# Optimization experiments

Measured on AMD Instinct MI355X. Metric: run time of the kernel, lower is better.

## Reference

```python
import jax, jax.numpy as jnp
import numpy as np

DIM = 768
NUM_HEADS = 12
HEAD_DIM = DIM // NUM_HEADS
SCALE = HEAD_DIM ** (-0.5)
LN_EPS = 1e-5


def setup_inputs() -> dict:
    key = jax.random.key(0)
    ks = jax.random.split(key, 8)
    B, K, C = 4, 2048, DIM
    return {
        "x": jax.random.normal(ks[0], (B, K, C), jnp.float32),
        "pos_embed": jax.random.normal(ks[1], (B, K, C), jnp.float32),
        "rel_pos_bias": jax.random.normal(ks[2], (B, K, K), jnp.float32),
        "ln_g": jnp.ones((C,), jnp.float32),
        "ln_b": jnp.zeros((C,), jnp.float32),
        "qkv_w": jax.random.normal(ks[3], (C, 3 * C), jnp.float32) * 0.02,
        "qkv_b": jnp.zeros((3 * C,), jnp.float32),
        "proj_w": jax.random.normal(ks[4], (C, C), jnp.float32) * 0.02,
        "proj_b": jnp.zeros((C,), jnp.float32),
    }


def _layernorm(x, g, b):
    mu = jnp.mean(x, axis=-1, keepdims=True)
    var = jnp.mean(jnp.square(x - mu), axis=-1, keepdims=True)
    return (x - mu) * jax.lax.rsqrt(var + LN_EPS) * g + b


def reference(x, pos_embed, rel_pos_bias, ln_g, ln_b, qkv_w, qkv_b, proj_w, proj_b):
    B, K, C = x.shape
    H, D = NUM_HEADS, HEAD_DIM
    xp = _layernorm(x, ln_g, ln_b) + pos_embed
    qkv = xp @ qkv_w + qkv_b                      # [B,K,3C]
    qkv = qkv.reshape(B, K, 3, H, D)
    q = jnp.transpose(qkv[:, :, 0], (0, 2, 1, 3))  # [B,H,K,D]
    k = jnp.transpose(qkv[:, :, 1], (0, 2, 1, 3))
    v = jnp.transpose(qkv[:, :, 2], (0, 2, 1, 3))
    attn = jnp.einsum("bhqd,bhkd->bhqk", q, k) * SCALE
    attn = attn + rel_pos_bias[:, None, :, :]
    attn = jax.nn.softmax(attn, axis=-1)
    out = jnp.einsum("bhqk,bhkd->bhqd", attn, v)   # [B,H,K,D]
    out = jnp.transpose(out, (0, 2, 1, 3)).reshape(B, K, C)
    # DropPath(0.1) is identity in eval mode
    return out @ proj_w + proj_b
```

## Files before the change

kernel.cpp:

```cpp
#include <hip/hip_runtime.h>
#include <hip/hip_bf16.h>
#include <stdint.h>

typedef __attribute__((ext_vector_type(4))) float f32x4;
typedef __attribute__((ext_vector_type(16))) float f32x16;
typedef __attribute__((ext_vector_type(8))) short s16x8;
typedef __attribute__((ext_vector_type(4))) short s16x4;
typedef uint16_t u16;

#define DEV __device__ __forceinline__

static DEV u16 f2bf(float f) {
  union { float f; uint32_t u; } v; v.f = f;
  uint32_t r = v.u + 0x7fffu + ((v.u >> 16) & 1u);
  return (u16)(r >> 16);
}

static DEV uint32_t cvt_pk_bf16(float lo, float hi) {
  uint32_t r;
  asm("v_cvt_pk_bf16_f32 %0, %1, %2" : "=v"(r) : "v"(lo), "v"(hi));
  return r;
}

#define GLD_LDS16(gp, lp) __builtin_amdgcn_global_load_lds( \
    (const __attribute__((address_space(1))) void*)(gp),    \
    (__attribute__((address_space(3))) void*)(lp), 16, 0, 0)

__global__ __launch_bounds__(256) void k_ln(
    const float* __restrict__ x, const float* __restrict__ pos,
    const float* __restrict__ g, const float* __restrict__ be,
    u16* __restrict__ xp) {
  int row = blockIdx.x;
  size_t base = (size_t)row * 768;
  int t = threadIdx.x;
  float v0 = x[base + t], v1 = x[base + t + 256], v2 = x[base + t + 512];
  float s = v0 + v1 + v2;
  float ss = v0 * v0 + v1 * v1 + v2 * v2;
#pragma unroll
  for (int off = 1; off < 64; off <<= 1) {
    s += __shfl_xor(s, off);
    ss += __shfl_xor(ss, off);
  }
  __shared__ float red[8];
  int wave = t >> 6, lane = t & 63;
  if (lane == 0) { red[wave] = s; red[4 + wave] = ss; }
  __syncthreads();
  float tot = red[0] + red[1] + red[2] + red[3];
  float tss = red[4] + red[5] + red[6] + red[7];
  float mu = tot * (1.0f / 768.0f);
  float var = tss * (1.0f / 768.0f) - mu * mu;
  float rs = rsqrtf(var + 1e-5f);
  float vv[3] = {v0, v1, v2};
#pragma unroll
  for (int i = 0; i < 3; ++i) {
    int c = t + i * 256;
    float val = (vv[i] - mu) * rs * g[c] + be[c] + pos[base + c];
    xp[base + c] = f2bf(val);
  }
}

__global__ __launch_bounds__(256) void k_tr(
    const float* __restrict__ in, u16* __restrict__ out, int K, int N) {
  __shared__ float tile[32][33];
  int n0 = blockIdx.x * 32, k0 = blockIdx.y * 32;
  int tx = threadIdx.x & 31, ty = threadIdx.x >> 5;
#pragma unroll
  for (int r = ty; r < 32; r += 8)
    tile[r][tx] = in[(size_t)(k0 + r) * N + n0 + tx];
  __syncthreads();
#pragma unroll
  for (int r = ty; r < 32; r += 8)
    out[(size_t)(n0 + r) * K + k0 + tx] = f2bf(tile[tx][r]);
}

__global__ __launch_bounds__(256) void k_gemm_qkv(
    const u16* __restrict__ A, const u16* __restrict__ Bt,
    const float* __restrict__ bias, u16* __restrict__ qkv,
    u16* __restrict__ vtg) {
  __shared__ u16 Al[128 * 64];
  __shared__ u16 Bl[128 * 64];
  const size_t BHKD = (size_t)48 * 2048 * 64;
  int mt = blockIdx.x, nt = blockIdx.y;
  int t = threadIdx.x, wave = t >> 6, lane = t & 63;
  int lr = lane & 15, lg = lane >> 4;
  f32x4 acc[4][4];
#pragma unroll
  for (int i = 0; i < 4; ++i)
#pragma unroll
    for (int j = 0; j < 4; ++j) acc[i][j] = (f32x4){0.f, 0.f, 0.f, 0.f};
  const size_t Ab = (size_t)mt * 128 * 768;
  const size_t Bb = (size_t)nt * 128 * 768;
  int wr = (wave >> 1) * 64, wc = (wave & 1) * 64;
  for (int kt = 0; kt < 12; ++kt) {
#pragma unroll
    for (int c = 0; c < 4; ++c) {
      int q = c * 256 + t;
      int row = q >> 3, ch = q & 7;
      int sc = ch ^ (row & 7);
      GLD_LDS16(A + Ab + (size_t)row * 768 + kt * 64 + sc * 8,
                &Al[(size_t)(c * 256 + wave * 64) * 8]);
      GLD_LDS16(Bt + Bb + (size_t)row * 768 + kt * 64 + sc * 8,
                &Bl[(size_t)(c * 256 + wave * 64) * 8]);
    }
    __syncthreads();
#pragma unroll
    for (int ki = 0; ki < 2; ++ki) {
      s16x8 af[4], bf[4];
#pragma unroll
      for (int mi = 0; mi < 4; ++mi)
        af[mi] = *(const s16x8*)&Al[(wr + mi * 16 + lr) * 64 +
                                    (((ki * 4 + lg) ^ (lr & 7)) * 8)];
#pragma unroll
      for (int ni = 0; ni < 4; ++ni)
        bf[ni] = *(const s16x8*)&Bl[(wc + ni * 16 + lr) * 64 +
                                    (((ki * 4 + lg) ^ (lr & 7)) * 8)];
#pragma unroll
      for (int mi = 0; mi < 4; ++mi)
#pragma unroll
        for (int ni = 0; ni < 4; ++ni)
          acc[mi][ni] = __builtin_amdgcn_mfma_f32_16x16x32_bf16(
              af[mi], bf[ni], acc[mi][ni], 0, 0, 0);
    }
    __syncthreads();
  }
#pragma unroll
  for (int ni = 0; ni < 4; ++ni) {
    int col = wc + ni * 16 + lr;
    int n = nt * 128 + col;
    int which = n / 768, cc = n % 768;
    int h = cc >> 6, d = cc & 63;
    float bs = bias[n];
    if (which == 2) {
#pragma unroll
      for (int mi = 0; mi < 4; ++mi) {
        int m0 = mt * 128 + wr + mi * 16 + lg * 4;
        int b = m0 >> 11, kp0 = m0 & 2047;
        s16x4 o4;
#pragma unroll
        for (int j = 0; j < 4; ++j) o4[j] = (short)f2bf(acc[mi][ni][j] + bs);
        *(s16x4*)&vtg[((size_t)(b * 12 + h) * 64 + d) * 2048 + kp0] = o4;
      }
    } else {
#pragma unroll
      for (int mi = 0; mi < 4; ++mi) {
#pragma unroll
        for (int j = 0; j < 4; ++j) {
          int row = wr + mi * 16 + lg * 4 + j;
          int m = mt * 128 + row;
          int b = m >> 11, kp = m & 2047;
          size_t dst = (size_t)which * BHKD +
                       (((size_t)b * 12 + h) * 2048 + kp) * 64 + d;
          qkv[dst] = f2bf(acc[mi][ni][j] + bs);
        }
      }
    }
  }
}

#define STAGE_KV(KB, VB, ktt) do {                                          \
  _Pragma("unroll")                                                         \
  for (int c_ = 0; c_ < 2; ++c_) {                                          \
    int q_ = c_ * 256 + t; int r_ = q_ >> 3, ch_ = q_ & 7;                  \
    int sc_ = ch_ ^ (r_ & 7);                                               \
    int gk_ = (r_ & 0x33) | ((r_ & 4) << 1) | ((r_ & 8) >> 1);              \
    GLD_LDS16(Kg + ((size_t)((ktt) * 64 + gk_)) * 64 + sc_ * 8,             \
              &KB[(c_ * 256 + wave * 64) * 8]);                             \
    GLD_LDS16(Vt + (size_t)r_ * 2048 + (ktt) * 64 + sc_ * 8,                \
              &VB[(c_ * 256 + wave * 64) * 8]);                             \
  }                                                                         \
} while (0)

#define COMPUTE_TILE(KB, VB, ktt) do {                                      \
  f32x4 bv_[8];                                                             \
  _Pragma("unroll")                                                         \
  for (int kv_ = 0; kv_ < 2; ++kv_) {                                       \
    _Pragma("unroll")                                                       \
    for (int rn_ = 0; rn_ < 2; ++rn_) {                                     \
      const float* bp_ = Bgl + (ktt) * 64 + kv_ * 32 + rn_ * 16;            \
      bv_[(kv_ * 2 + rn_) * 2]     = *(const f32x4*)bp_;                    \
      bv_[(kv_ * 2 + rn_) * 2 + 1] = *(const f32x4*)(bp_ + 4);              \
    }                                                                       \
  }                                                                         \
  f32x16 sa_[2];                                                            \
  _Pragma("unroll")                                                         \
  for (int r = 0; r < 16; ++r) { sa_[0][r] = 0.f; sa_[1][r] = 0.f; }        \
  _Pragma("unroll")                                                         \
  for (int ki = 0; ki < 4; ++ki) {                                          \
    _Pragma("unroll")                                                       \
    for (int kv_ = 0; kv_ < 2; ++kv_) {                                     \
      s16x8 kf = *(const s16x8*)&KB[(kv_ * 32 + l31) * 64 +                 \
                                    (((ki * 2 + hi) ^ (l31 & 7)) * 8)];     \
      sa_[kv_] = __builtin_amdgcn_mfma_f32_32x32x16_bf16(kf, qf[ki],        \
                                                         sa_[kv_], 0, 0, 0);\
    }                                                                       \
  }                                                                         \
  float p_[32];                                                             \
  _Pragma("unroll")                                                         \
  for (int kv_ = 0; kv_ < 2; ++kv_)                                         \
    _Pragma("unroll")                                                       \
    for (int r = 0; r < 16; ++r)                                            \
      p_[kv_ * 16 + r] = exp2f(                                             \
          __builtin_fmaf(sa_[kv_][r], 0.125f,                               \
              bv_[kv_ * 4 + (r >> 3) * 2 + ((r >> 2) & 1)][r & 3]) *        \
          1.442695041f);                                                    \
  float tm_[16];                                                            \
  _Pragma("unroll")                                                         \
  for (int i = 0; i < 16; ++i) tm_[i] = p_[i] + p_[i + 16];                 \
  _Pragma("unroll")                                                         \
  for (int off = 8; off >= 1; off >>= 1)                                    \
    _Pragma("unroll")                                                       \
    for (int i = 0; i < off; ++i) tm_[i] += tm_[i + off];                   \
  l_run += tm_[0];                                                          \
  union { uint32_t u[4]; s16x8 v; } pa_[4];                                 \
  _Pragma("unroll")                                                         \
  for (int s = 0; s < 4; ++s)                                               \
    _Pragma("unroll")                                                       \
    for (int w = 0; w < 4; ++w)                                             \
      pa_[s].u[w] = cvt_pk_bf16(p_[(s >> 1) * 16 + (s & 1) * 8 + 2 * w],    \
                                p_[(s >> 1) * 16 + (s & 1) * 8 + 2 * w + 1]);\
  _Pragma("unroll")                                                         \
  for (int s = 0; s < 4; ++s) {                                             \
    _Pragma("unroll")                                                       \
    for (int dt = 0; dt < 2; ++dt) {                                        \
      s16x8 vf = *(const s16x8*)&VB[(dt * 32 + l31) * 64 +                  \
                                    (((s * 2 + hi) ^ (l31 & 7)) * 8)];      \
      oacc[dt] = __builtin_amdgcn_mfma_f32_32x32x16_bf16(vf, pa_[s].v,      \
                                                         oacc[dt], 0, 0, 0);\
    }                                                                       \
  }                                                                         \
} while (0)

__global__ __launch_bounds__(256, 3) void k_attn(
    const u16* __restrict__ qkv, const u16* __restrict__ vtg,
    const float* __restrict__ bias, u16* __restrict__ ctx) {
  __shared__ u16 Kl0[64 * 64], Vl0[64 * 64];
  __shared__ u16 Kl1[64 * 64], Vl1[64 * 64];
  int bid = blockIdx.x;
  int swz = (bid & 7) * 96 + (bid >> 3);
  int h = swz % 12;
  int bq = swz / 12;
  int qt = bq & 15;
  int b = bq >> 4;
  int bh = b * 12 + h;
  int t = threadIdx.x, wave = t >> 6, lane = t & 63;
  int l31 = lane & 31, hi = lane >> 5;
  const size_t BHKD = (size_t)48 * 2048 * 64;
  const u16* Q = qkv + (size_t)bh * 2048 * 64;
  const u16* Kg = Q + BHKD;
  const u16* Vt = vtg + (size_t)bh * 64 * 2048;
  int qrow = qt * 128 + wave * 32 + l31;
  const float* Bgl = bias + ((size_t)b * 2048 + qrow) * 2048 + hi * 8;
  s16x8 qf[4];
#pragma unroll
  for (int ki = 0; ki < 4; ++ki)
    qf[ki] = *(const s16x8*)&Q[(size_t)qrow * 64 + ki * 16 + hi * 8];
  f32x16 oacc[2];
#pragma unroll
  for (int r = 0; r < 16; ++r) { oacc[0][r] = 0.f; oacc[1][r] = 0.f; }
  float l_run = 0.f;

  STAGE_KV(Kl0, Vl0, 0);
  __syncthreads();
  for (int kt = 0; kt < 32; kt += 2) {
    STAGE_KV(Kl1, Vl1, kt + 1);
    COMPUTE_TILE(Kl0, Vl0, kt);
    __syncthreads();
    if (kt + 2 < 32) STAGE_KV(Kl0, Vl0, kt + 2);
    COMPUTE_TILE(Kl1, Vl1, kt + 1);
    __syncthreads();
  }
  float l_tot = l_run + __shfl_xor(l_run, 32);
  float inv = 1.0f / l_tot;
  size_t obase = ((size_t)b * 2048 + qrow) * 768 + h * 64;
#pragma unroll
  for (int dt = 0; dt < 2; ++dt) {
#pragma unroll
    for (int g = 0; g < 4; ++g) {
      s16x4 o4;
#pragma unroll
      for (int j = 0; j < 4; ++j)
        o4[j] = (short)f2bf(oacc[dt][g * 4 + j] * inv);
      *(s16x4*)&ctx[obase + dt * 32 + g * 8 + hi * 4] = o4;
    }
  }
}

__global__ __launch_bounds__(256) void k_gemm_proj(
    const u16* __restrict__ A, const u16* __restrict__ Bt,
    const float* __restrict__ bias, float* __restrict__ out) {
  __shared__ u16 Al[128 * 64];
  __shared__ u16 Bl[128 * 64];
  int mt = blockIdx.x, nt = blockIdx.y;
  int t = threadIdx.x, wave = t >> 6, lane = t & 63;
  int lr = lane & 15, lg = lane >> 4;
  f32x4 acc[4][4];
#pragma unroll
  for (int i = 0; i < 4; ++i)
#pragma unroll
    for (int j = 0; j < 4; ++j) acc[i][j] = (f32x4){0.f, 0.f, 0.f, 0.f};
  const size_t Ab = (size_t)mt * 128 * 768;
  const size_t Bb = (size_t)nt * 128 * 768;
  int wr = (wave >> 1) * 64, wc = (wave & 1) * 64;
  for (int kt = 0; kt < 12; ++kt) {
#pragma unroll
    for (int c = 0; c < 4; ++c) {
      int q = c * 256 + t;
      int row = q >> 3, ch = q & 7;
      int sc = ch ^ (row & 7);
      GLD_LDS16(A + Ab + (size_t)row * 768 + kt * 64 + sc * 8,
                &Al[(size_t)(c * 256 + wave * 64) * 8]);
      GLD_LDS16(Bt + Bb + (size_t)row * 768 + kt * 64 + sc * 8,
                &Bl[(size_t)(c * 256 + wave * 64) * 8]);
    }
    __syncthreads();
#pragma unroll
    for (int ki = 0; ki < 2; ++ki) {
      s16x8 af[4], bf[4];
#pragma unroll
      for (int mi = 0; mi < 4; ++mi)
        af[mi] = *(const s16x8*)&Al[(wr + mi * 16 + lr) * 64 +
                                    (((ki * 4 + lg) ^ (lr & 7)) * 8)];
#pragma unroll
      for (int ni = 0; ni < 4; ++ni)
        bf[ni] = *(const s16x8*)&Bl[(wc + ni * 16 + lr) * 64 +
                                    (((ki * 4 + lg) ^ (lr & 7)) * 8)];
#pragma unroll
      for (int mi = 0; mi < 4; ++mi)
#pragma unroll
        for (int ni = 0; ni < 4; ++ni)
          acc[mi][ni] = __builtin_amdgcn_mfma_f32_16x16x32_bf16(
              af[mi], bf[ni], acc[mi][ni], 0, 0, 0);
    }
    __syncthreads();
  }
#pragma unroll
  for (int ni = 0; ni < 4; ++ni) {
    int col = wc + ni * 16 + lr;
    int n = nt * 128 + col;
    float bs = bias[n];
#pragma unroll
    for (int mi = 0; mi < 4; ++mi) {
#pragma unroll
      for (int j = 0; j < 4; ++j) {
        int row = wr + mi * 16 + lg * 4 + j;
        out[(size_t)(mt * 128 + row) * 768 + n] = acc[mi][ni][j] + bs;
      }
    }
  }
}

extern "C" void kernel_launch(void* const* d_in, const int* in_sizes, int n_in,
                              void* d_out, int out_size, void* d_ws, size_t ws_size,
                              hipStream_t stream) {
  const float* x      = (const float*)d_in[0];
  const float* pos    = (const float*)d_in[1];
  const float* bias   = (const float*)d_in[2];
  const float* ln_g   = (const float*)d_in[3];
  const float* ln_b   = (const float*)d_in[4];
  const float* qkv_w  = (const float*)d_in[5];
  const float* qkv_b  = (const float*)d_in[6];
  const float* proj_w = (const float*)d_in[7];
  const float* proj_b = (const float*)d_in[8];
  float* out = (float*)d_out;

  char* ws = (char*)d_ws;
  u16* xp      = (u16*)ws;              ws += 12582912;
  u16* qkv_wt  = (u16*)ws;              ws += 3538944;
  u16* proj_wt = (u16*)ws;              ws += 1179648;
  u16* qkvbuf  = (u16*)ws;              ws += 25165824;
  u16* ctx     = (u16*)ws;              ws += 12582912;
  u16* vtg     = (u16*)ws;              ws += 12582912;

  k_ln<<<8192, 256, 0, stream>>>(x, pos, ln_g, ln_b, xp);
  k_tr<<<dim3(72, 24), 256, 0, stream>>>(qkv_w, qkv_wt, 768, 2304);
  k_tr<<<dim3(24, 24), 256, 0, stream>>>(proj_w, proj_wt, 768, 768);
  k_gemm_qkv<<<dim3(64, 18), 256, 0, stream>>>(xp, qkv_wt, qkv_b, qkvbuf, vtg);
  k_attn<<<768, 256, 0, stream>>>(qkvbuf, vtg, bias, ctx);
  k_gemm_proj<<<dim3(64, 6), 256, 0, stream>>>(ctx, proj_wt, proj_b, out);
}
```

Baseline: 205.0 us.

## Load K/V fragments directly from global memory instead of staging through LDS

Removes the double-buffered LDS staging of K and V tiles and their barriers in the attention kernel. Each lane now reads its MFMA K and V fragments straight from global memory, relying on L1/L2 reuse across the four waves that share the same K/V tile. This eliminates LDS traffic and __syncthreads, but each wave issues its own global loads, so cache-level traffic is up to 4x higher and latency is only hidden by within-iteration ordering. The occupancy hint of 3 blocks per CU is also dropped.

Result: slower. 346.7 us (+69.1%).

```diff
diff --git a/kernel.cpp b/kernel.cpp
--- a/kernel.cpp
+++ b/kernel.cpp
@@ -157,84 +157,9 @@
   }
 }
 
-#define STAGE_KV(KB, VB, ktt) do {                                          \
-  _Pragma("unroll")                                                         \
-  for (int c_ = 0; c_ < 2; ++c_) {                                          \
-    int q_ = c_ * 256 + t; int r_ = q_ >> 3, ch_ = q_ & 7;                  \
-    int sc_ = ch_ ^ (r_ & 7);                                               \
-    int gk_ = (r_ & 0x33) | ((r_ & 4) << 1) | ((r_ & 8) >> 1);              \
-    GLD_LDS16(Kg + ((size_t)((ktt) * 64 + gk_)) * 64 + sc_ * 8,             \
-              &KB[(c_ * 256 + wave * 64) * 8]);                             \
-    GLD_LDS16(Vt + (size_t)r_ * 2048 + (ktt) * 64 + sc_ * 8,                \
-              &VB[(c_ * 256 + wave * 64) * 8]);                             \
-  }                                                                         \
-} while (0)
-
-#define COMPUTE_TILE(KB, VB, ktt) do {                                      \
-  f32x4 bv_[8];                                                             \
-  _Pragma("unroll")                                                         \
-  for (int kv_ = 0; kv_ < 2; ++kv_) {                                       \
-    _Pragma("unroll")                                                       \
-    for (int rn_ = 0; rn_ < 2; ++rn_) {                                     \
-      const float* bp_ = Bgl + (ktt) * 64 + kv_ * 32 + rn_ * 16;            \
-      bv_[(kv_ * 2 + rn_) * 2]     = *(const f32x4*)bp_;                    \
-      bv_[(kv_ * 2 + rn_) * 2 + 1] = *(const f32x4*)(bp_ + 4);              \
-    }                                                                       \
-  }                                                                         \
-  f32x16 sa_[2];                                                            \
-  _Pragma("unroll")                                                         \
-  for (int r = 0; r < 16; ++r) { sa_[0][r] = 0.f; sa_[1][r] = 0.f; }        \
-  _Pragma("unroll")                                                         \
-  for (int ki = 0; ki < 4; ++ki) {                                          \
-    _Pragma("unroll")                                                       \
-    for (int kv_ = 0; kv_ < 2; ++kv_) {                                     \
-      s16x8 kf = *(const s16x8*)&KB[(kv_ * 32 + l31) * 64 +                 \
-                                    (((ki * 2 + hi) ^ (l31 & 7)) * 8)];     \
-      sa_[kv_] = __builtin_amdgcn_mfma_f32_32x32x16_bf16(kf, qf[ki],        \
-                                                         sa_[kv_], 0, 0, 0);\
-    }                                                                       \
-  }                                                                         \
-  float p_[32];                                                             \
-  _Pragma("unroll")                                                         \
-  for (int kv_ = 0; kv_ < 2; ++kv_)                                         \
-    _Pragma("unroll")                                                       \
-    for (int r = 0; r < 16; ++r)                                            \
-      p_[kv_ * 16 + r] = exp2f(                                             \
-          __builtin_fmaf(sa_[kv_][r], 0.125f,                               \
-              bv_[kv_ * 4 + (r >> 3) * 2 + ((r >> 2) & 1)][r & 3]) *        \
-          1.442695041f);                                                    \
-  float tm_[16];                                                            \
-  _Pragma("unroll")                                                         \
-  for (int i = 0; i < 16; ++i) tm_[i] = p_[i] + p_[i + 16];                 \
-  _Pragma("unroll")                                                         \
-  for (int off = 8; off >= 1; off >>= 1)                                    \
-    _Pragma("unroll")                                                       \
-    for (int i = 0; i < off; ++i) tm_[i] += tm_[i + off];                   \
-  l_run += tm_[0];                                                          \
-  union { uint32_t u[4]; s16x8 v; } pa_[4];                                 \
-  _Pragma("unroll")                                                         \
-  for (int s = 0; s < 4; ++s)                                               \
-    _Pragma("unroll")                                                       \
-    for (int w = 0; w < 4; ++w)                                             \
-      pa_[s].u[w] = cvt_pk_bf16(p_[(s >> 1) * 16 + (s & 1) * 8 + 2 * w],    \
-                                p_[(s >> 1) * 16 + (s & 1) * 8 + 2 * w + 1]);\
-  _Pragma("unroll")                                                         \
-  for (int s = 0; s < 4; ++s) {                                             \
-    _Pragma("unroll")                                                       \
-    for (int dt = 0; dt < 2; ++dt) {                                        \
-      s16x8 vf = *(const s16x8*)&VB[(dt * 32 + l31) * 64 +                  \
-                                    (((s * 2 + hi) ^ (l31 & 7)) * 8)];      \
-      oacc[dt] = __builtin_amdgcn_mfma_f32_32x32x16_bf16(vf, pa_[s].v,      \
-                                                         oacc[dt], 0, 0, 0);\
-    }                                                                       \
-  }                                                                         \
-} while (0)
-
-__global__ __launch_bounds__(256, 3) void k_attn(
+__global__ __launch_bounds__(256) void k_attn(
     const u16* __restrict__ qkv, const u16* __restrict__ vtg,
     const float* __restrict__ bias, u16* __restrict__ ctx) {
-  __shared__ u16 Kl0[64 * 64], Vl0[64 * 64];
-  __shared__ u16 Kl1[64 * 64], Vl1[64 * 64];
   int bid = blockIdx.x;
   int swz = (bid & 7) * 96 + (bid >> 3);
   int h = swz % 12;
@@ -244,12 +169,15 @@
   int bh = b * 12 + h;
   int t = threadIdx.x, wave = t >> 6, lane = t & 63;
   int l31 = lane & 31, hi = lane >> 5;
+  int l31s = (l31 & 0x13) | ((l31 & 4) << 1) | ((l31 & 8) >> 1);
   const size_t BHKD = (size_t)48 * 2048 * 64;
   const u16* Q = qkv + (size_t)bh * 2048 * 64;
   const u16* Kg = Q + BHKD;
   const u16* Vt = vtg + (size_t)bh * 64 * 2048;
   int qrow = qt * 128 + wave * 32 + l31;
   const float* Bgl = bias + ((size_t)b * 2048 + qrow) * 2048 + hi * 8;
+  const u16* Kp0 = Kg + (size_t)l31s * 64 + hi * 8;
+  const u16* Vp0 = Vt + (size_t)l31 * 2048 + hi * 8;
   s16x8 qf[4];
 #pragma unroll
   for (int ki = 0; ki < 4; ++ki)
@@ -259,15 +187,71 @@
   for (int r = 0; r < 16; ++r) { oacc[0][r] = 0.f; oacc[1][r] = 0.f; }
   float l_run = 0.f;
 
-  STAGE_KV(Kl0, Vl0, 0);
-  __syncthreads();
-  for (int kt = 0; kt < 32; kt += 2) {
-    STAGE_KV(Kl1, Vl1, kt + 1);
-    COMPUTE_TILE(Kl0, Vl0, kt);
-    __syncthreads();
-    if (kt + 2 < 32) STAGE_KV(Kl0, Vl0, kt + 2);
-    COMPUTE_TILE(Kl1, Vl1, kt + 1);
-    __syncthreads();
+#pragma unroll 1
+  for (int kt = 0; kt < 32; ++kt) {
+    f32x4 bv_[8];
+#pragma unroll
+    for (int kv2 = 0; kv2 < 2; ++kv2) {
+#pragma unroll
+      for (int rn = 0; rn < 2; ++rn) {
+        const float* bp_ = Bgl + kt * 64 + kv2 * 32 + rn * 16;
+        bv_[(kv2 * 2 + rn) * 2]     = *(const f32x4*)bp_;
+        bv_[(kv2 * 2 + rn) * 2 + 1] = *(const f32x4*)(bp_ + 4);
+      }
+    }
+    s16x8 kf[8];
+#pragma unroll
+    for (int ki = 0; ki < 4; ++ki)
+#pragma unroll
+      for (int kv2 = 0; kv2 < 2; ++kv2)
+        kf[ki * 2 + kv2] = *(const s16x8*)(Kp0 +
+            ((size_t)kt * 64 + kv2 * 32) * 64 + ki * 16);
+    f32x16 sa_[2];
+#pragma unroll
+    for (int r = 0; r < 16; ++r) { sa_[0][r] = 0.f; sa_[1][r] = 0.f; }
+#pragma unroll
+    for (int ki = 0; ki < 4; ++ki)
+#pragma unroll
+      for (int kv2 = 0; kv2 < 2; ++kv2)
+        sa_[kv2] = __builtin_amdgcn_mfma_f32_32x32x16_bf16(
+            kf[ki * 2 + kv2], qf[ki], sa_[kv2], 0, 0, 0);
+    s16x8 vf[8];
+#pragma unroll
+    for (int s = 0; s < 4; ++s)
+#pragma unroll
+      for (int dt = 0; dt < 2; ++dt)
+        vf[s * 2 + dt] = *(const s16x8*)(Vp0 +
+            (size_t)dt * 32 * 2048 + kt * 64 + s * 16);
+    float p_[32];
+#pragma unroll
+    for (int kv2 = 0; kv2 < 2; ++kv2)
+#pragma unroll
+      for (int r = 0; r < 16; ++r)
+        p_[kv2 * 16 + r] = exp2f(
+            __builtin_fmaf(sa_[kv2][r], 0.125f,
+                bv_[kv2 * 4 + (r >> 3) * 2 + ((r >> 2) & 1)][r & 3]) *
+            1.442695041f);
+    float tm_[16];
+#pragma unroll
+    for (int i = 0; i < 16; ++i) tm_[i] = p_[i] + p_[i + 16];
+#pragma unroll
+    for (int off = 8; off >= 1; off >>= 1)
+#pragma unroll
+      for (int i = 0; i < off; ++i) tm_[i] += tm_[i + off];
+    l_run += tm_[0];
+    union { uint32_t u[4]; s16x8 v; } pa_[4];
+#pragma unroll
+    for (int s = 0; s < 4; ++s)
+#pragma unroll
+      for (int w = 0; w < 4; ++w)
+        pa_[s].u[w] = cvt_pk_bf16(p_[(s >> 1) * 16 + (s & 1) * 8 + 2 * w],
+                                  p_[(s >> 1) * 16 + (s & 1) * 8 + 2 * w + 1]);
+#pragma unroll
+    for (int s = 0; s < 4; ++s)
+#pragma unroll
+      for (int dt = 0; dt < 2; ++dt)
+        oacc[dt] = __builtin_amdgcn_mfma_f32_32x32x16_bf16(
+            vf[s * 2 + dt], pa_[s].v, oacc[dt], 0, 0, 0);
   }
   float l_tot = l_run + __shfl_xor(l_run, 32);
   float inv = 1.0f / l_tot;
```

## Split attention KV tile across two wave groups and reduce partials via LDS

Applied to the files above, without the earlier changes.

The attention block grows from 256 to 512 threads. Each group of four waves handles half of every 64-key tile, so per-wave score, exp and PV work is halved, and staging is spread over twice as many threads. The two partial outputs and row sums are combined through shared memory at the end before normalising. The goal is more waves in flight to hide latency, at the cost of extra LDS (about 17 KB), extra barriers and a final reduction, with fewer blocks able to reside per CU.

New measurement: 402.8 us. +96.5%, slower.

```diff
diff --git a/kernel.cpp b/kernel.cpp
--- a/kernel.cpp
+++ b/kernel.cpp
@@ -158,83 +158,71 @@
 }
 
 #define STAGE_KV(KB, VB, ktt) do {                                          \
-  _Pragma("unroll")                                                         \
-  for (int c_ = 0; c_ < 2; ++c_) {                                          \
-    int q_ = c_ * 256 + t; int r_ = q_ >> 3, ch_ = q_ & 7;                  \
+    int r_ = t >> 3, ch_ = t & 7;                                           \
     int sc_ = ch_ ^ (r_ & 7);                                               \
     int gk_ = (r_ & 0x33) | ((r_ & 4) << 1) | ((r_ & 8) >> 1);              \
     GLD_LDS16(Kg + ((size_t)((ktt) * 64 + gk_)) * 64 + sc_ * 8,             \
-              &KB[(c_ * 256 + wave * 64) * 8]);                             \
+              &KB[wave * 64 * 8]);                                          \
     GLD_LDS16(Vt + (size_t)r_ * 2048 + (ktt) * 64 + sc_ * 8,                \
-              &VB[(c_ * 256 + wave * 64) * 8]);                             \
+              &VB[wave * 64 * 8]);                                          \
+} while (0)
+
+#define COMPUTE_TILE(KB, VB, ktt) do {                                      \
+  f32x4 bv_[4];                                                             \
+  {                                                                         \
+    const float* bp_ = Bgl + (ktt) * 64 + kvh * 32;                         \
+    bv_[0] = *(const f32x4*)bp_;                                            \
+    bv_[1] = *(const f32x4*)(bp_ + 4);                                      \
+    bv_[2] = *(const f32x4*)(bp_ + 16);                                     \
+    bv_[3] = *(const f32x4*)(bp_ + 20);                                     \
   }                                                                         \
-} while (0)
-
-#define COMPUTE_TILE(KB, VB, ktt) do {                                      \
-  f32x4 bv_[8];                                                             \
-  _Pragma("unroll")                                                         \
-  for (int kv_ = 0; kv_ < 2; ++kv_) {                                       \
-    _Pragma("unroll")                                                       \
-    for (int rn_ = 0; rn_ < 2; ++rn_) {                                     \
-      const float* bp_ = Bgl + (ktt) * 64 + kv_ * 32 + rn_ * 16;            \
-      bv_[(kv_ * 2 + rn_) * 2]     = *(const f32x4*)bp_;                    \
-      bv_[(kv_ * 2 + rn_) * 2 + 1] = *(const f32x4*)(bp_ + 4);              \
-    }                                                                       \
+  f32x16 sa_;                                                               \
+  _Pragma("unroll")                                                         \
+  for (int r = 0; r < 16; ++r) sa_[r] = 0.f;                                \
+  _Pragma("unroll")                                                         \
+  for (int ki = 0; ki < 4; ++ki) {                                          \
+    s16x8 kf = *(const s16x8*)&KB[(kvh * 32 + l31) * 64 +                   \
+                                  (((ki * 2 + hi) ^ (l31 & 7)) * 8)];       \
+    sa_ = __builtin_amdgcn_mfma_f32_32x32x16_bf16(kf, qf[ki], sa_, 0, 0, 0);\
   }                                                                         \
-  f32x16 sa_[2];                                                            \
-  _Pragma("unroll")                                                         \
-  for (int r = 0; r < 16; ++r) { sa_[0][r] = 0.f; sa_[1][r] = 0.f; }        \
-  _Pragma("unroll")                                                         \
-  for (int ki = 0; ki < 4; ++ki) {                                          \
-    _Pragma("unroll")                                                       \
-    for (int kv_ = 0; kv_ < 2; ++kv_) {                                     \
-      s16x8 kf = *(const s16x8*)&KB[(kv_ * 32 + l31) * 64 +                 \
-                                    (((ki * 2 + hi) ^ (l31 & 7)) * 8)];     \
-      sa_[kv_] = __builtin_amdgcn_mfma_f32_32x32x16_bf16(kf, qf[ki],        \
-                                                         sa_[kv_], 0, 0, 0);\
-    }                                                                       \
-  }                                                                         \
-  float p_[32];                                                             \
-  _Pragma("unroll")                                                         \
-  for (int kv_ = 0; kv_ < 2; ++kv_)                                         \
-    _Pragma("unroll")                                                       \
-    for (int r = 0; r < 16; ++r)                                            \
-      p_[kv_ * 16 + r] = exp2f(                                             \
-          __builtin_fmaf(sa_[kv_][r], 0.125f,                               \
-              bv_[kv_ * 4 + (r >> 3) * 2 + ((r >> 2) & 1)][r & 3]) *        \
-          1.442695041f);                                                    \
-  float tm_[16];                                                            \
-  _Pragma("unroll")                                                         \
-  for (int i = 0; i < 16; ++i) tm_[i] = p_[i] + p_[i + 16];                 \
-  _Pragma("unroll")                                                         \
-  for (int off = 8; off >= 1; off >>= 1)                                    \
+  float p_[16];                                                             \
+  _Pragma("unroll")                                                         \
+  for (int r = 0; r < 16; ++r)                                              \
+    p_[r] = exp2f(__builtin_fmaf(sa_[r], 0.125f,                            \
+                bv_[(r >> 3) * 2 + ((r >> 2) & 1)][r & 3]) * 1.442695041f); \
+  float tm_[8];                                                             \
+  _Pragma("unroll")                                                         \
+  for (int i = 0; i < 8; ++i) tm_[i] = p_[i] + p_[i + 8];                   \
+  _Pragma("unroll")                                                         \
+  for (int off = 4; off >= 1; off >>= 1)                                    \
     _Pragma("unroll")                                                       \
     for (int i = 0; i < off; ++i) tm_[i] += tm_[i + off];                   \
   l_run += tm_[0];                                                          \
-  union { uint32_t u[4]; s16x8 v; } pa_[4];                                 \
-  _Pragma("unroll")                                                         \
-  for (int s = 0; s < 4; ++s)                                               \
+  union { uint32_t u[4]; s16x8 v; } pa_[2];                                 \
+  _Pragma("unroll")                                                         \
+  for (int s = 0; s < 2; ++s)                                               \
     _Pragma("unroll")                                                       \
     for (int w = 0; w < 4; ++w)                                             \
-      pa_[s].u[w] = cvt_pk_bf16(p_[(s >> 1) * 16 + (s & 1) * 8 + 2 * w],    \
-                                p_[(s >> 1) * 16 + (s & 1) * 8 + 2 * w + 1]);\
-  _Pragma("unroll")                                                         \
-  for (int s = 0; s < 4; ++s) {                                             \
+      pa_[s].u[w] = cvt_pk_bf16(p_[s * 8 + 2 * w], p_[s * 8 + 2 * w + 1]);  \
+  _Pragma("unroll")                                                         \
+  for (int s = 0; s < 2; ++s) {                                             \
     _Pragma("unroll")                                                       \
     for (int dt = 0; dt < 2; ++dt) {                                        \
       s16x8 vf = *(const s16x8*)&VB[(dt * 32 + l31) * 64 +                  \
-                                    (((s * 2 + hi) ^ (l31 & 7)) * 8)];      \
+                    (((kvh * 4 + s * 2 + hi) ^ (l31 & 7)) * 8)];            \
       oacc[dt] = __builtin_amdgcn_mfma_f32_32x32x16_bf16(vf, pa_[s].v,      \
                                                          oacc[dt], 0, 0, 0);\
     }                                                                       \
   }                                                                         \
 } while (0)
 
-__global__ __launch_bounds__(256, 3) void k_attn(
+__global__ __launch_bounds__(512, 6) void k_attn(
     const u16* __restrict__ qkv, const u16* __restrict__ vtg,
     const float* __restrict__ bias, u16* __restrict__ ctx) {
   __shared__ u16 Kl0[64 * 64], Vl0[64 * 64];
   __shared__ u16 Kl1[64 * 64], Vl1[64 * 64];
+  __shared__ float Cb[4 * 64 * 16];
+  __shared__ float Lb[4 * 64];
   int bid = blockIdx.x;
   int swz = (bid & 7) * 96 + (bid >> 3);
   int h = swz % 12;
@@ -244,11 +232,12 @@
   int bh = b * 12 + h;
   int t = threadIdx.x, wave = t >> 6, lane = t & 63;
   int l31 = lane & 31, hi = lane >> 5;
+  int qg = wave & 3, kvh = wave >> 2;
   const size_t BHKD = (size_t)48 * 2048 * 64;
   const u16* Q = qkv + (size_t)bh * 2048 * 64;
   const u16* Kg = Q + BHKD;
   const u16* Vt = vtg + (size_t)bh * 64 * 2048;
-  int qrow = qt * 128 + wave * 32 + l31;
+  int qrow = qt * 128 + qg * 32 + l31;
   const float* Bgl = bias + ((size_t)b * 2048 + qrow) * 2048 + hi * 8;
   s16x8 qf[4];
 #pragma unroll
@@ -269,18 +258,40 @@
     COMPUTE_TILE(Kl1, Vl1, kt + 1);
     __syncthreads();
   }
-  float l_tot = l_run + __shfl_xor(l_run, 32);
-  float inv = 1.0f / l_tot;
-  size_t obase = ((size_t)b * 2048 + qrow) * 768 + h * 64;
-#pragma unroll
-  for (int dt = 0; dt < 2; ++dt) {
-#pragma unroll
-    for (int g = 0; g < 4; ++g) {
-      s16x4 o4;
-#pragma unroll
-      for (int j = 0; j < 4; ++j)
-        o4[j] = (short)f2bf(oacc[dt][g * 4 + j] * inv);
-      *(s16x4*)&ctx[obase + dt * 32 + g * 8 + hi * 4] = o4;
+  if (wave >= 4) {
+    Lb[qg * 64 + lane] = l_run;
+#pragma unroll
+    for (int j = 0; j < 16; ++j) Cb[(qg * 64 + lane) * 16 + j] = oacc[0][j];
+  }
+  __syncthreads();
+  float l_tot = 1.f;
+  if (wave < 4) {
+    float lsum = l_run + Lb[qg * 64 + lane];
+    l_tot = lsum + __shfl_xor(lsum, 32);
+#pragma unroll
+    for (int j = 0; j < 16; ++j) oacc[0][j] += Cb[(qg * 64 + lane) * 16 + j];
+  }
+  __syncthreads();
+  if (wave >= 4) {
+#pragma unroll
+    for (int j = 0; j < 16; ++j) Cb[(qg * 64 + lane) * 16 + j] = oacc[1][j];
+  }
+  __syncthreads();
+  if (wave < 4) {
+#pragma unroll
+    for (int j = 0; j < 16; ++j) oacc[1][j] += Cb[(qg * 64 + lane) * 16 + j];
+    float inv = 1.0f / l_tot;
+    size_t obase = ((size_t)b * 2048 + qrow) * 768 + h * 64;
+#pragma unroll
+    for (int dt = 0; dt < 2; ++dt) {
+#pragma unroll
+      for (int g = 0; g < 4; ++g) {
+        s16x4 o4;
+#pragma unroll
+        for (int j = 0; j < 4; ++j)
+          o4[j] = (short)f2bf(oacc[dt][g * 4 + j] * inv);
+        *(s16x4*)&ctx[obase + dt * 32 + g * 8 + hi * 4] = o4;
+      }
     }
   }
 }
@@ -375,6 +386,6 @@
   k_tr<<<dim3(72, 24), 256, 0, stream>>>(qkv_w, qkv_wt, 768, 2304);
   k_tr<<<dim3(24, 24), 256, 0, stream>>>(proj_w, proj_wt, 768, 768);
   k_gemm_qkv<<<dim3(64, 18), 256, 0, stream>>>(xp, qkv_wt, qkv_b, qkvbuf, vtg);
-  k_attn<<<768, 256, 0, stream>>>(qkvbuf, vtg, bias, ctx);
+  k_attn<<<768, 512, 0, stream>>>(qkvbuf, vtg, bias, ctx);
   k_gemm_proj<<<dim3(64, 6), 256, 0, stream>>>(ctx, proj_wt, proj_b, out);
 }
```

## Split attention key range across two blocks and combine partials in a separate kernel

Applied to the files above, without the earlier changes.

Each attention block now processes only half of the key tiles, doubling the grid from 768 to 1536 blocks. Each block writes unnormalized bf16 partial outputs and per-row softmax denominators. A new combine kernel sums the two halves and normalizes them into ctx. This aims to raise parallelism and reduce per-block latency, at the cost of an extra kernel launch, extra global traffic for the partial buffers, and bf16 rounding of the partials before they are summed.

Measured after the change: 219.8 us. 1.07x slower.

```diff
diff --git a/kernel.cpp b/kernel.cpp
--- a/kernel.cpp
+++ b/kernel.cpp
@@ -14,6 +14,11 @@
   union { float f; uint32_t u; } v; v.f = f;
   uint32_t r = v.u + 0x7fffu + ((v.u >> 16) & 1u);
   return (u16)(r >> 16);
+}
+
+static DEV float bf2f(u16 x) {
+  union { uint32_t u; float f; } v; v.u = ((uint32_t)x) << 16;
+  return v.f;
 }
 
 static DEV uint32_t cvt_pk_bf16(float lo, float hi) {
@@ -232,13 +237,16 @@
 
 __global__ __launch_bounds__(256, 3) void k_attn(
     const u16* __restrict__ qkv, const u16* __restrict__ vtg,
-    const float* __restrict__ bias, u16* __restrict__ ctx) {
+    const float* __restrict__ bias, u16* __restrict__ opart,
+    float* __restrict__ lpart) {
   __shared__ u16 Kl0[64 * 64], Vl0[64 * 64];
   __shared__ u16 Kl1[64 * 64], Vl1[64 * 64];
   int bid = blockIdx.x;
-  int swz = (bid & 7) * 96 + (bid >> 3);
+  int swz = (bid & 7) * 192 + (bid >> 3);
   int h = swz % 12;
-  int bq = swz / 12;
+  int tmp = swz / 12;
+  int half = tmp & 1;
+  int bq = tmp >> 1;
   int qt = bq & 15;
   int b = bq >> 4;
   int bh = b * 12 + h;
@@ -258,19 +266,22 @@
 #pragma unroll
   for (int r = 0; r < 16; ++r) { oacc[0][r] = 0.f; oacc[1][r] = 0.f; }
   float l_run = 0.f;
-
-  STAGE_KV(Kl0, Vl0, 0);
+  int kt0 = half * 16;
+
+  STAGE_KV(Kl0, Vl0, kt0);
   __syncthreads();
-  for (int kt = 0; kt < 32; kt += 2) {
-    STAGE_KV(Kl1, Vl1, kt + 1);
-    COMPUTE_TILE(Kl0, Vl0, kt);
-    __syncthreads();
-    if (kt + 2 < 32) STAGE_KV(Kl0, Vl0, kt + 2);
-    COMPUTE_TILE(Kl1, Vl1, kt + 1);
-    __syncthreads();
-  }
-  float l_tot = l_run + __shfl_xor(l_run, 32);
-  float inv = 1.0f / l_tot;
+  for (int kt = 0; kt < 16; kt += 2) {
+    STAGE_KV(Kl1, Vl1, kt0 + kt + 1);
+    COMPUTE_TILE(Kl0, Vl0, kt0 + kt);
+    __syncthreads();
+    if (kt + 2 < 16) STAGE_KV(Kl0, Vl0, kt0 + kt + 2);
+    COMPUTE_TILE(Kl1, Vl1, kt0 + kt + 1);
+    __syncthreads();
+  }
+  float l_half = l_run + __shfl_xor(l_run, 32);
+  int p = (bh * 16 + qt) * 2 + half;
+  if (hi == 0) lpart[p * 128 + wave * 32 + l31] = l_half;
+  u16* op = opart + (size_t)half * 8192 * 768;
   size_t obase = ((size_t)b * 2048 + qrow) * 768 + h * 64;
 #pragma unroll
   for (int dt = 0; dt < 2; ++dt) {
@@ -279,9 +290,32 @@
       s16x4 o4;
 #pragma unroll
       for (int j = 0; j < 4; ++j)
-        o4[j] = (short)f2bf(oacc[dt][g * 4 + j] * inv);
-      *(s16x4*)&ctx[obase + dt * 32 + g * 8 + hi * 4] = o4;
-    }
+        o4[j] = (short)f2bf(oacc[dt][g * 4 + j]);
+      *(s16x4*)&op[obase + dt * 32 + g * 8 + hi * 4] = o4;
+    }
+  }
+}
+
+__global__ __launch_bounds__(256) void k_comb(
+    const u16* __restrict__ opart, const float* __restrict__ lpart,
+    u16* __restrict__ ctx) {
+  int qt = blockIdx.x, bh = blockIdx.y;
+  int b = bh / 12, h = bh - b * 12;
+  int t = threadIdx.x;
+  int q = t >> 1, dh = (t & 1) * 32;
+  int p = (bh * 16 + qt) * 2;
+  float inv = 1.0f / (lpart[p * 128 + q] + lpart[(p + 1) * 128 + q]);
+  const size_t HSZ = (size_t)8192 * 768;
+  size_t base = ((size_t)(b * 2048 + qt * 128 + q)) * 768 + h * 64 + dh;
+#pragma unroll
+  for (int c = 0; c < 4; ++c) {
+    s16x8 a = *(const s16x8*)&opart[base + c * 8];
+    s16x8 bb = *(const s16x8*)&opart[HSZ + base + c * 8];
+    s16x8 o;
+#pragma unroll
+    for (int i = 0; i < 8; ++i)
+      o[i] = (short)f2bf((bf2f((u16)a[i]) + bf2f((u16)bb[i])) * inv);
+    *(s16x8*)&ctx[base + c * 8] = o;
   }
 }
 
@@ -370,11 +404,14 @@
   u16* qkvbuf  = (u16*)ws;              ws += 25165824;
   u16* ctx     = (u16*)ws;              ws += 12582912;
   u16* vtg     = (u16*)ws;              ws += 12582912;
+  u16* opart   = (u16*)ws;              ws += 25165824;
+  float* lpart = (float*)ws;            ws += 786432;
 
   k_ln<<<8192, 256, 0, stream>>>(x, pos, ln_g, ln_b, xp);
   k_tr<<<dim3(72, 24), 256, 0, stream>>>(qkv_w, qkv_wt, 768, 2304);
   k_tr<<<dim3(24, 24), 256, 0, stream>>>(proj_w, proj_wt, 768, 768);
   k_gemm_qkv<<<dim3(64, 18), 256, 0, stream>>>(xp, qkv_wt, qkv_b, qkvbuf, vtg);
-  k_attn<<<768, 256, 0, stream>>>(qkvbuf, vtg, bias, ctx);
+  k_attn<<<1536, 256, 0, stream>>>(qkvbuf, vtg, bias, opart, lpart);
+  k_comb<<<dim3(16, 48), 256, 0, stream>>>(opart, lpart, ctx);
   k_gemm_proj<<<dim3(64, 6), 256, 0, stream>>>(ctx, proj_wt, proj_b, out);
 }
```
